# Optimization experiments

Hardware: AMD Instinct MI355X
Metric: run time of the kernel (lower is better)

The kernel has to match this reference:

```python
import jax, jax.numpy as jnp
import numpy as np

D_MODEL = 512
D_STATE = 64
D_CONV = 4
EXPAND = 2
D_INNER = EXPAND * D_MODEL  # 1024
DT_RANK = D_MODEL // 16     # 32 (mamba default: ceil(d_model/16))
BATCH = 1
SEQ = 2048


def setup_inputs() -> dict:
    key = jax.random.key(0)
    ks = jax.random.split(key, 10)
    def n(k, shape, scale):
        return jax.random.normal(k, shape, dtype=jnp.float32) * scale
    x = n(ks[0], (BATCH, SEQ, D_MODEL), 1.0)
    ln_g = jnp.ones((D_MODEL,), jnp.float32)
    ln_b = jnp.zeros((D_MODEL,), jnp.float32)
    Win = n(ks[1], (2 * D_INNER, D_MODEL), D_MODEL ** -0.5)
    conv_w = n(ks[2], (D_INNER, 1, D_CONV), 0.5)      # depthwise kernel (O,I/g,K)
    conv_b = n(ks[3], (D_INNER,), 0.02)
    Wx = n(ks[4], (DT_RANK + 2 * D_STATE, D_INNER), D_INNER ** -0.5)
    Wdt = n(ks[5], (D_INNER, DT_RANK), DT_RANK ** -0.5)
    bdt = n(ks[6], (D_INNER,), 0.02)
    # Mamba S4D-real init: A = 1..d_state repeated per channel
    A_log = jnp.log(jnp.tile(jnp.arange(1, D_STATE + 1, dtype=jnp.float32)[None, :], (D_INNER, 1)))
    Dp = jnp.ones((D_INNER,), jnp.float32)
    Wout = n(ks[7], (D_MODEL, D_INNER), D_INNER ** -0.5)
    return dict(x=x, ln_g=ln_g, ln_b=ln_b, Win=Win, conv_w=conv_w, conv_b=conv_b,
                Wx=Wx, Wdt=Wdt, bdt=bdt, A_log=A_log, Dp=Dp, Wout=Wout)


def _layernorm(x, g, b, eps=1e-5):
    mu = jnp.mean(x, axis=-1, keepdims=True)
    xc = x - mu
    var = jnp.mean(xc * xc, axis=-1, keepdims=True)
    return xc * jax.lax.rsqrt(var + eps) * g + b


def _mamba_block(x, ln_g, ln_b, Win, conv_w, conv_b, Wx, Wdt, bdt, A_log, Dp, Wout):
    residual = x
    xn = _layernorm(x, ln_g, ln_b)
    # in_proj -> (x, z) gates
    xz = jnp.einsum('bld,ed->ble', xn, Win)           # (B,L,2*D_INNER)
    xi, z = jnp.split(xz, 2, axis=-1)
    # causal depthwise conv1d (torch pads d_conv-1 both sides then truncates to L == left-pad only)
    xc = jnp.transpose(xi, (0, 2, 1))                 # (B,C,L)
    xc = jax.lax.conv_general_dilated(
        xc, conv_w, window_strides=(1,), padding=[(D_CONV - 1, 0)],
        dimension_numbers=('NCH', 'OIH', 'NCH'), feature_group_count=D_INNER)
    xc = xc + conv_b[None, :, None]
    xi = jax.nn.silu(jnp.transpose(xc, (0, 2, 1)))    # (B,L,D_INNER)
    # x_proj -> dt, B, C
    dbc = jnp.einsum('bld,ed->ble', xi, Wx)           # (B,L,DT_RANK+2N)
    dt = dbc[..., :DT_RANK]
    Bm = dbc[..., DT_RANK:DT_RANK + D_STATE]          # (B,L,N)
    Cm = dbc[..., DT_RANK + D_STATE:]                 # (B,L,N)
    delta = jax.nn.softplus(jnp.einsum('blr,dr->bld', dt, Wdt) + bdt)  # (B,L,D_INNER)
    A = -jnp.exp(A_log)                               # (D_INNER,N), negative
    dA = jnp.exp(delta[..., None] * A)                # (B,L,D_INNER,N) in (0,1)
    dBx = (delta * xi)[..., None] * Bm[:, :, None, :] # (B,L,D_INNER,N)
    def step(h, t):
        dA_t, dBx_t, C_t = t
        h = dA_t * h + dBx_t                          # (B,D_INNER,N)
        y_t = jnp.einsum('bdn,bn->bd', h, C_t)
        return h, y_t
    h0 = jnp.zeros((x.shape[0], D_INNER, D_STATE), x.dtype)
    _, ys = jax.lax.scan(step, h0, (jnp.transpose(dA, (1, 0, 2, 3)),
                                    jnp.transpose(dBx, (1, 0, 2, 3)),
                                    jnp.transpose(Cm, (1, 0, 2))))
    y = jnp.transpose(ys, (1, 0, 2)) + Dp * xi        # skip term D*x
    y = y * jax.nn.silu(z)                            # gate
    out = jnp.einsum('bld,ed->ble', y, Wout)          # out_proj
    return out + residual


def reference(x, ln_g, ln_b, Win, conv_w, conv_b, Wx, Wdt, bdt, A_log, Dp, Wout):
    return _mamba_block(x, ln_g, ln_b, Win, conv_w, conv_b, Wx, Wdt, bdt, A_log, Dp, Wout)
```

## Files before the change

### kernel.cpp

```cpp
#include <hip/hip_runtime.h>
#include <hip/hip_bf16.h>
#include <cstddef>

#define SEQ 2048
#define DM  512
#define DI  1024
#define DR  32
#define DS  64
#define NCHUNK 32
#define CHUNK  64
#define MB (1024 * 1024)
#define NCVT 1696

typedef __attribute__((ext_vector_type(4))) float f32x4;
typedef __attribute__((ext_vector_type(2))) float f32x2;
typedef __attribute__((ext_vector_type(8))) short frag8;

__device__ __forceinline__ unsigned short f2bf(float f) {
    unsigned u = __float_as_uint(f);
    unsigned r = (u + 0x7fffu + ((u >> 16) & 1u)) >> 16;
    return (unsigned short)r;
}
__device__ __forceinline__ float bf2f(unsigned short u) {
    return __int_as_float(((int)u) << 16);
}

__device__ __forceinline__ float fexp2(float x) {
#if __has_builtin(__builtin_amdgcn_exp2f)
    return __builtin_amdgcn_exp2f(x);
#else
    return exp2f(x);
#endif
}
#define LOG2E 1.44269504088896f

template <int CTRL>
__device__ __forceinline__ f32x2 dppadd2(f32x2 p) {
    f32x2 t;
    t.x = __int_as_float(
        __builtin_amdgcn_update_dpp(0, __float_as_int(p.x), CTRL, 0xF, 0xF, true));
    t.y = __int_as_float(
        __builtin_amdgcn_update_dpp(0, __float_as_int(p.y), CTRL, 0xF, 0xF, true));
    return p + t;
}

__global__ void cvt_ln(const float* __restrict__ w1, unsigned short* __restrict__ o1,
                       const float* __restrict__ w2, unsigned short* __restrict__ o2,
                       const float* __restrict__ w3, unsigned short* __restrict__ o3,
                       const float* __restrict__ x, const float* __restrict__ g,
                       const float* __restrict__ b, unsigned short* __restrict__ xn) {
    if (blockIdx.x < NCVT) {
        const int n1 = 1048576, n2 = 163840, n3 = 524288;
        int i = (blockIdx.x * 256 + threadIdx.x) * 4;
        const float* s; unsigned short* d; int off;
        if (i < n1) { s = w1; d = o1; off = i; }
        else if (i < n1 + n2) { s = w2; d = o2; off = i - n1; }
        else if (i < n1 + n2 + n3) { s = w3; d = o3; off = i - n1 - n2; }
        else return;
        float4 v = *(const float4*)(s + off);
        ushort4 o = { f2bf(v.x), f2bf(v.y), f2bf(v.z), f2bf(v.w) };
        *(ushort4*)(d + off) = o;
        return;
    }
    int l = blockIdx.x - NCVT;
    int t = threadIdx.x;
    __shared__ float red[256];
    float v0 = x[l * DM + t];
    float v1 = x[l * DM + t + 256];
    red[t] = v0 + v1;
    __syncthreads();
    for (int o = 128; o > 0; o >>= 1) { if (t < o) red[t] += red[t + o]; __syncthreads(); }
    float mu = red[0] * (1.f / DM);
    __syncthreads();
    float c0 = v0 - mu, c1 = v1 - mu;
    red[t] = c0 * c0 + c1 * c1;
    __syncthreads();
    for (int o = 128; o > 0; o >>= 1) { if (t < o) red[t] += red[t + o]; __syncthreads(); }
    float rstd = rsqrtf(red[0] * (1.f / DM) + 1e-5f);
    xn[l * DM + t]       = f2bf(c0 * rstd * g[t]       + b[t]);
    xn[l * DM + t + 256] = f2bf(c1 * rstd * g[t + 256] + b[t + 256]);
}

#define LDK 40

template <int EPI>
__global__ __launch_bounds__(256, 2)
void gemm_bf(const unsigned short* __restrict__ A, int lda,
             const unsigned short* __restrict__ B, int ldb,
             int N, int K,
             float* __restrict__ outF, const float* __restrict__ res, int ldo,
             float* __restrict__ dtc, float* __restrict__ Bfp, float* __restrict__ Cfp,
             unsigned short* __restrict__ outB1, unsigned short* __restrict__ outB2) {
    __shared__ unsigned short As[128 * LDK];
    __shared__ unsigned short Bs[64 * LDK];
    int t = threadIdx.x;
    int lane = t & 63;
    int wv = t >> 6;
    int wm = (wv >> 1) * 64;
    int wn = (wv & 1) * 32;
    int m0 = blockIdx.x * 128, n0 = blockIdx.y * 64;

    f32x4 acc[4][2];
#pragma unroll
    for (int i = 0; i < 4; i++)
#pragma unroll
        for (int j = 0; j < 2; j++) acc[i][j] = (f32x4){0.f, 0.f, 0.f, 0.f};

    int lm = lane & 15;
    int kq = (lane >> 4) * 8;

    for (int k0 = 0; k0 < K; k0 += 32) {
#pragma unroll
        for (int j = 0; j < 2; j++) {
            int c = t + j * 256;
            int m = c >> 2;
            int k = (c & 3) * 8;
            frag8 v = *(const frag8*)(A + (size_t)(m0 + m) * lda + k0 + k);
            *(frag8*)(&As[m * LDK + k]) = v;
        }
        {
            int m = t >> 2;
            int k = (t & 3) * 8;
            int gn = n0 + m;
            frag8 v = {0, 0, 0, 0, 0, 0, 0, 0};
            if (gn < N) v = *(const frag8*)(B + (size_t)gn * ldb + k0 + k);
            *(frag8*)(&Bs[m * LDK + k]) = v;
        }
        __syncthreads();

        frag8 af[4], bfr[2];
#pragma unroll
        for (int mt = 0; mt < 4; mt++)
            af[mt] = *(const frag8*)(&As[(wm + mt * 16 + lm) * LDK + kq]);
#pragma unroll
        for (int nt = 0; nt < 2; nt++)
            bfr[nt] = *(const frag8*)(&Bs[(wn + nt * 16 + lm) * LDK + kq]);
#pragma unroll
        for (int mt = 0; mt < 4; mt++)
#pragma unroll
            for (int nt = 0; nt < 2; nt++)
                acc[mt][nt] = __builtin_amdgcn_mfma_f32_16x16x32_bf16(
                    af[mt], bfr[nt], acc[mt][nt], 0, 0, 0);
        __syncthreads();
    }

    int rbase = (lane >> 4) * 4;
#pragma unroll
    for (int mt = 0; mt < 4; mt++) {
#pragma unroll
        for (int nt = 0; nt < 2; nt++) {
            int n = n0 + wn + nt * 16 + lm;
            int mb = m0 + wm + mt * 16 + rbase;
            if (EPI == 1) {
                if (n < DI) {
#pragma unroll
                    for (int r = 0; r < 4; r++)
                        outB1[(size_t)(mb + r) * DI + n] = f2bf(acc[mt][nt][r]);
                } else {
                    int nn = n - DI;
                    ushort4 o;
#pragma unroll
                    for (int r = 0; r < 4; r++) {
                        float v = acc[mt][nt][r];
                        v = v / (1.f + __expf(-v));
                        (&o.x)[r] = f2bf(v);
                    }
                    *(ushort4*)(outB2 + (size_t)nn * SEQ + mb) = o;
                }
            } else if (EPI == 2) {
                if (n < N) {
#pragma unroll
                    for (int r = 0; r < 4; r++)
                        outF[(size_t)(mb + r) * ldo + n] =
                            acc[mt][nt][r] + res[(size_t)(mb + r) * ldo + n];
                }
            } else {
                if (n < 32) {
#pragma unroll
                    for (int r = 0; r < 4; r++)
                        dtc[(size_t)(mb + r) * 32 + n] = acc[mt][nt][r];
                } else if (n < 96) {
#pragma unroll
                    for (int r = 0; r < 4; r++)
                        Bfp[(size_t)(mb + r) * DS + (n - 32)] = acc[mt][nt][r];
                } else if (n < 160) {
#pragma unroll
                    for (int r = 0; r < 4; r++)
                        Cfp[(size_t)(mb + r) * DS + (n - 96)] = acc[mt][nt][r];
                }
            }
        }
    }
}

__global__ void gemm_dt_t(const float* __restrict__ A,
                          const float* __restrict__ B,
                          const float* __restrict__ bias,
                          float* __restrict__ outT) {
    __shared__ float As[16][65];
    __shared__ float Bs[16][65];
    int tid = threadIdx.x;
    int tx = tid & 15, ty = tid >> 4;
    int bm = blockIdx.x * 64, bn = blockIdx.y * 64;
    float acc[4][4] = {};
    int kk = tid & 15;
    int rr = tid >> 4;
    for (int k0 = 0; k0 < DR; k0 += 16) {
#pragma unroll
        for (int i = 0; i < 4; i++)
            As[kk][rr + 16 * i] = A[(size_t)(bm + rr + 16 * i) * 32 + k0 + kk];
#pragma unroll
        for (int i = 0; i < 4; i++)
            Bs[kk][rr + 16 * i] = B[(size_t)(bn + rr + 16 * i) * DR + k0 + kk];
        __syncthreads();
#pragma unroll
        for (int k = 0; k < 16; k++) {
            float a[4], bb[4];
#pragma unroll
            for (int i = 0; i < 4; i++) a[i] = As[k][ty * 4 + i];
#pragma unroll
            for (int j = 0; j < 4; j++) bb[j] = Bs[k][tx * 4 + j];
#pragma unroll
            for (int i = 0; i < 4; i++)
#pragma unroll
                for (int j = 0; j < 4; j++)
                    acc[i][j] = fmaf(a[i], bb[j], acc[i][j]);
        }
        __syncthreads();
    }
#pragma unroll
    for (int j = 0; j < 4; j++) {
        int e = bn + tx * 4 + j;
        float bv = bias[e];
        float4 o;
#pragma unroll
        for (int i = 0; i < 4; i++) {
            float v = acc[i][j] + bv;
            v = (v > 20.f) ? v : __logf(1.f + __expf(v));
            (&o.x)[i] = v;
        }
        *(float4*)(outT + (size_t)e * SEQ + bm + ty * 4) = o;
    }
}

__global__ void conv_t(const unsigned short* __restrict__ xi_raw,
                       const float* __restrict__ w, const float* __restrict__ cb,
                       unsigned short* __restrict__ xi2bf, unsigned short* __restrict__ xi2T) {
    __shared__ float tin[67][72];
    __shared__ float tout[64][65];
    int l0 = blockIdx.x * 64, e0 = blockIdx.y * 64;
    int t = threadIdx.x;
    for (int c = t; c < 536; c += 256) {
        int r = c >> 3, ke = (c & 7) * 8;
        int l = l0 - 3 + r;
        frag8 v = {0, 0, 0, 0, 0, 0, 0, 0};
        if (l >= 0) v = *(const frag8*)(xi_raw + (size_t)l * DI + e0 + ke);
#pragma unroll
        for (int i = 0; i < 8; i++) tin[r][ke + i] = bf2f((unsigned short)v[i]);
    }
    __syncthreads();
    int e_loc = t & 63;
    int e = e0 + e_loc;
    float4 wv = *(const float4*)(w + e * 4);
    float bias = cb[e];
#pragma unroll 4
    for (int i = 0; i < 16; i++) {
        int l_loc = (t >> 6) + i * 4;
        float acc = bias;
        acc = fmaf(wv.x, tin[l_loc][e_loc], acc);
        acc = fmaf(wv.y, tin[l_loc + 1][e_loc], acc);
        acc = fmaf(wv.z, tin[l_loc + 2][e_loc], acc);
        acc = fmaf(wv.w, tin[l_loc + 3][e_loc], acc);
        float s = acc / (1.f + __expf(-acc));
        tout[l_loc][e_loc] = s;
        xi2bf[(size_t)(l0 + l_loc) * DI + e] = f2bf(s);
    }
    __syncthreads();
    for (int c = t; c < 1024; c += 256) {
        int er = c >> 4, l4 = (c & 15) * 4;
        ushort4 o = { f2bf(tout[l4][er]), f2bf(tout[l4 + 1][er]),
                      f2bf(tout[l4 + 2][er]), f2bf(tout[l4 + 3][er]) };
        *(ushort4*)(xi2T + (size_t)(e0 + er) * SEQ + l0 + l4) = o;
    }
}

struct GrpA { float4 dd; ushort4 xx; float4 B[4]; };
struct GrpB { float4 dd; ushort4 xx, zz; float4 B[4], C[4]; };

__device__ __forceinline__ void loadGrpA(GrpA& gr, const float4* d4, const ushort4* x4,
                                         const float4* b4, int gq) {
    gr.dd = d4[gq]; gr.xx = x4[gq];
#pragma unroll
    for (int j = 0; j < 4; j++) gr.B[j] = b4[(4 * gq + j) * 16];
}

__device__ __forceinline__ void loadGrpB(GrpB& gr, const float4* d4, const ushort4* x4,
                                         const ushort4* s4, const float4* b4,
                                         const float4* c4, int gq) {
    gr.dd = d4[gq]; gr.xx = x4[gq]; gr.zz = s4[gq];
#pragma unroll
    for (int j = 0; j < 4; j++) {
        gr.B[j] = b4[(4 * gq + j) * 16];
        gr.C[j] = c4[(4 * gq + j) * 16];
    }
}

__device__ __forceinline__ void compGrpA(const GrpA& gr, f32x2& h01, f32x2& h23,
                                         float& sum_d, f32x2 nA01, f32x2 nA23) {
#pragma unroll
    for (int j = 0; j < 4; j++) {
        float dj = (&gr.dd.x)[j];
        f32x2 dj2 = {dj, dj};
        f32x2 e01 = dj2 * nA01, e23 = dj2 * nA23;
        f32x2 dA01, dA23;
        dA01.x = fexp2(e01.x); dA01.y = fexp2(e01.y);
        dA23.x = fexp2(e23.x); dA23.y = fexp2(e23.y);
        float dx = dj * bf2f((&gr.xx.x)[j]);
        f32x2 dx2 = {dx, dx};
        sum_d += dj;
        f32x2 B01 = {gr.B[j].x, gr.B[j].y}, B23 = {gr.B[j].z, gr.B[j].w};
        h01 = dA01 * h01 + dx2 * B01;
        h23 = dA23 * h23 + dx2 * B23;
    }
}

__device__ __forceinline__ void compGrpB(const GrpB& gr, f32x2& h01, f32x2& h23,
                                         f32x2 nA01, f32x2 nA23, float dp, int i,
                                         size_t ybase, unsigned short* __restrict__ y_bf) {
    float ps[4], xs[4];
#pragma unroll
    for (int j = 0; j < 4; j++) {
        float dj = (&gr.dd.x)[j];
        f32x2 dj2 = {dj, dj};
        f32x2 e01 = dj2 * nA01, e23 = dj2 * nA23;
        f32x2 dA01, dA23;
        dA01.x = fexp2(e01.x); dA01.y = fexp2(e01.y);
        dA23.x = fexp2(e23.x); dA23.y = fexp2(e23.y);
        float xj = bf2f((&gr.xx.x)[j]);
        float dx = dj * xj;
        f32x2 dx2 = {dx, dx};
        f32x2 B01 = {gr.B[j].x, gr.B[j].y}, B23 = {gr.B[j].z, gr.B[j].w};
        h01 = dA01 * h01 + dx2 * B01;
        h23 = dA23 * h23 + dx2 * B23;
        f32x2 C01 = {gr.C[j].x, gr.C[j].y}, C23 = {gr.C[j].z, gr.C[j].w};
        f32x2 pp = h01 * C01;
        pp = h23 * C23 + pp;
        ps[j] = pp.x + pp.y;
        xs[j] = xj;
    }
    f32x2 q01 = {ps[0], ps[1]}, q23 = {ps[2], ps[3]};
    q01 = dppadd2<0xB1>(q01);  q23 = dppadd2<0xB1>(q23);
    q01 = dppadd2<0x4E>(q01);  q23 = dppadd2<0x4E>(q23);
    q01 = dppadd2<0x141>(q01); q23 = dppadd2<0x141>(q23);
    q01 = dppadd2<0x140>(q01); q23 = dppadd2<0x140>(q23);
    f32x2 x01 = {xs[0], xs[1]}, x23 = {xs[2], xs[3]};
    f32x2 z01 = {bf2f(gr.zz.x), bf2f(gr.zz.y)}, z23 = {bf2f(gr.zz.z), bf2f(gr.zz.w)};
    f32x2 dp2 = {dp, dp};
    f32x2 y01 = (q01 + dp2 * x01) * z01;
    f32x2 y23 = (q23 + dp2 * x23) * z23;
    if (i == 0) {
        y_bf[ybase]          = f2bf(y01.x);
        y_bf[ybase + DI]     = f2bf(y01.y);
        y_bf[ybase + 2 * DI] = f2bf(y23.x);
        y_bf[ybase + 3 * DI] = f2bf(y23.y);
    }
}

__global__ __launch_bounds__(256, 4)
void scan_passA(const float* __restrict__ deltaT, const unsigned short* __restrict__ xi2T,
                const float* __restrict__ Bf, const float* __restrict__ A_log,
                float* __restrict__ sumd, float* __restrict__ hend) {
    __shared__ float Bsh[CHUNK * DS];
    int t = threadIdx.x;
    int wid = blockIdx.x * 4 + (t >> 6);
    int eg = wid & 255;
    int c  = wid >> 8;
    int l0 = c * CHUNK;
#pragma unroll
    for (int it = 0; it < 4; it++) {
        int idx = (it * 256 + t) * 4;
        *(float4*)&Bsh[idx] = *(const float4*)(Bf + (size_t)l0 * DS + idx);
    }
    __syncthreads();
    int lane = t & 63;
    int g = lane >> 4;
    int i = lane & 15;
    int e = eg * 4 + g;
    float4 al = *(const float4*)(A_log + e * DS + 4 * i);
    f32x2 nA01 = { -__expf(al.x) * LOG2E, -__expf(al.y) * LOG2E };
    f32x2 nA23 = { -__expf(al.z) * LOG2E, -__expf(al.w) * LOG2E };
    f32x2 h01 = {0.f, 0.f}, h23 = {0.f, 0.f};
    float sum_d = 0.f;
    const float4* d4  = (const float4*)(deltaT + (size_t)e * SEQ + l0);
    const ushort4* x4 = (const ushort4*)(xi2T + (size_t)e * SEQ + l0);
    const float4* b4  = (const float4*)Bsh + i;
    GrpA ga, gb;
    loadGrpA(ga, d4, x4, b4, 0);
    for (int p = 0; p < CHUNK / 8; p++) {
        loadGrpA(gb, d4, x4, b4, 2 * p + 1);
        compGrpA(ga, h01, h23, sum_d, nA01, nA23);
        if (p < CHUNK / 8 - 1) loadGrpA(ga, d4, x4, b4, 2 * p + 2);
        compGrpA(gb, h01, h23, sum_d, nA01, nA23);
    }
    size_t idx = ((size_t)c * DI + e) * DS + 4 * i;
    float4 hv = {h01.x, h01.y, h23.x, h23.y};
    *(float4*)(hend + idx) = hv;
    if (i == 0) sumd[c * DI + e] = sum_d;
}

__global__ void scan_carry(float* __restrict__ hend, const float* __restrict__ sumd,
                           const float* __restrict__ A_log) {
    int e = blockIdx.x * 4 + (threadIdx.x >> 6);
    int n = threadIdx.x & 63;
    float Ae2 = -__expf(A_log[e * DS + n]) * LOG2E;
    float he[NCHUNK - 1], sd[NCHUNK - 1];
#pragma unroll
    for (int c = 0; c < NCHUNK - 1; c++)
        he[c] = hend[((size_t)c * DI + e) * DS + n];
#pragma unroll
    for (int c = 0; c < NCHUNK - 1; c++)
        sd[c] = sumd[c * DI + e];
    float h = 0.f;
#pragma unroll
    for (int c = 0; c < NCHUNK - 1; c++) {
        float P = fexp2(Ae2 * sd[c]);
        hend[((size_t)c * DI + e) * DS + n] = h;
        h = fmaf(P, h, he[c]);
    }
    hend[((size_t)(NCHUNK - 1) * DI + e) * DS + n] = h;
}

__global__ __launch_bounds__(256, 4)
void scan_passB(const float* __restrict__ deltaT, const unsigned short* __restrict__ xi2T,
                const float* __restrict__ Bf, const float* __restrict__ Cf,
                const unsigned short* __restrict__ szT,
                const float* __restrict__ A_log, const float* __restrict__ Dp,
                const float* __restrict__ hin, unsigned short* __restrict__ y_bf) {
    __shared__ float Bsh[CHUNK * DS];
    __shared__ float Csh[CHUNK * DS];
    int t = threadIdx.x;
    int wid = blockIdx.x * 4 + (t >> 6);
    int eg = wid & 255;
    int c  = wid >> 8;
    int l0 = c * CHUNK;
#pragma unroll
    for (int it = 0; it < 4; it++) {
        int idx = (it * 256 + t) * 4;
        *(float4*)&Bsh[idx] = *(const float4*)(Bf + (size_t)l0 * DS + idx);
        *(float4*)&Csh[idx] = *(const float4*)(Cf + (size_t)l0 * DS + idx);
    }
    __syncthreads();
    int lane = t & 63;
    int g = lane >> 4;
    int i = lane & 15;
    int e = eg * 4 + g;
    float4 al = *(const float4*)(A_log + e * DS + 4 * i);
    f32x2 nA01 = { -__expf(al.x) * LOG2E, -__expf(al.y) * LOG2E };
    f32x2 nA23 = { -__expf(al.z) * LOG2E, -__expf(al.w) * LOG2E };
    float dp = Dp[e];
    float4 hv = *(const float4*)(hin + ((size_t)c * DI + e) * DS + 4 * i);
    f32x2 h01 = {hv.x, hv.y}, h23 = {hv.z, hv.w};
    const float4* d4  = (const float4*)(deltaT + (size_t)e * SEQ + l0);
    const ushort4* x4 = (const ushort4*)(xi2T + (size_t)e * SEQ + l0);
    const ushort4* s4 = (const ushort4*)(szT + (size_t)e * SEQ + l0);
    const float4* b4  = (const float4*)Bsh + i;
    const float4* c4  = (const float4*)Csh + i;
    size_t ybase = (size_t)l0 * DI + e;
    GrpB ga, gb;
    loadGrpB(ga, d4, x4, s4, b4, c4, 0);
    for (int p = 0; p < CHUNK / 8; p++) {
        loadGrpB(gb, d4, x4, s4, b4, c4, 2 * p + 1);
        compGrpB(ga, h01, h23, nA01, nA23, dp, i, ybase + (size_t)(8 * p) * DI, y_bf);
        if (p < CHUNK / 8 - 1) loadGrpB(ga, d4, x4, s4, b4, c4, 2 * p + 2);
        compGrpB(gb, h01, h23, nA01, nA23, dp, i, ybase + (size_t)(8 * p + 4) * DI, y_bf);
    }
}

extern "C" void kernel_launch(void* const* d_in, const int* in_sizes, int n_in,
                              void* d_out, int out_size, void* d_ws, size_t ws_size,
                              hipStream_t stream) {
    const float* x      = (const float*)d_in[0];
    const float* ln_g   = (const float*)d_in[1];
    const float* ln_b   = (const float*)d_in[2];
    const float* Win    = (const float*)d_in[3];
    const float* conv_w = (const float*)d_in[4];
    const float* conv_b = (const float*)d_in[5];
    const float* Wx     = (const float*)d_in[6];
    const float* Wdt    = (const float*)d_in[7];
    const float* bdt    = (const float*)d_in[8];
    const float* A_log  = (const float*)d_in[9];
    const float* Dp     = (const float*)d_in[10];
    const float* Wout   = (const float*)d_in[11];
    float* out = (float*)d_out;

    char* W = (char*)d_ws;
    unsigned short* xi_raw  = (unsigned short*)W;
    float*          deltaT  = (float*)W;
    unsigned short* Win_bf  = (unsigned short*)(W + 8 * MB);
    unsigned short* xi2bf   = (unsigned short*)(W + 8 * MB);
    unsigned short* y_bf    = (unsigned short*)(W + 8 * MB);
    unsigned short* szT     = (unsigned short*)(W + 12 * MB);
    unsigned short* xi2T    = (unsigned short*)(W + 16 * MB);
    unsigned short* xn_bf   = (unsigned short*)(W + 20 * MB);
    float*          hend    = (float*)(W + 20 * MB);
    unsigned short* Wout_bf = (unsigned short*)(W + 28 * MB);
    float*          sumd    = (float*)(W + 29 * MB);
    unsigned short* Wx_bf   = (unsigned short*)(W + 29 * MB + 128 * 1024);
    float*          dtc     = (float*)(W + 29 * MB + 448 * 1024);
    float*          Bf      = (float*)(W + 29 * MB + 704 * 1024);
    float*          Cf      = Bf + (size_t)SEQ * DS;

    cvt_ln<<<NCVT + SEQ, 256, 0, stream>>>(Win, Win_bf, Wx, Wx_bf, Wout, Wout_bf,
                                           x, ln_g, ln_b, xn_bf);

    gemm_bf<1><<<dim3(SEQ / 128, 2048 / 64), 256, 0, stream>>>(
        xn_bf, DM, Win_bf, DM, 2048, DM, nullptr, nullptr, 0, nullptr, nullptr, nullptr,
        xi_raw, szT);

    conv_t<<<dim3(SEQ / 64, DI / 64), 256, 0, stream>>>(xi_raw, conv_w, conv_b, xi2bf, xi2T);

    gemm_bf<4><<<dim3(SEQ / 128, 3), 256, 0, stream>>>(
        xi2bf, DI, Wx_bf, DI, 160, DI, nullptr, nullptr, 0, dtc, Bf, Cf, nullptr, nullptr);

    gemm_dt_t<<<dim3(SEQ / 64, DI / 64), 256, 0, stream>>>(dtc, Wdt, bdt, deltaT);

    scan_passA<<<(DI / 4) * (NCHUNK - 1) / 4, 256, 0, stream>>>(deltaT, xi2T, Bf, A_log, sumd, hend);
    scan_carry<<<DI / 4, 256, 0, stream>>>(hend, sumd, A_log);
    scan_passB<<<(DI / 4) * NCHUNK / 4, 256, 0, stream>>>(deltaT, xi2T, Bf, Cf, szT,
                                                          A_log, Dp, hend, y_bf);

    gemm_bf<2><<<dim3(SEQ / 128, DM / 64), 256, 0, stream>>>(
        y_bf, DI, Wout_bf, DI, DM, DI, out, x, DM, nullptr, nullptr, nullptr,
        nullptr, nullptr);
}
```

Measured before the change: 219.7 us.

## Double-buffer GEMM tiles with direct global-to-LDS loads and pad Wx weights

The bf16 GEMM now stages A and B tiles straight from global memory into LDS with global_load_lds, using two LDS buffers so the next K-slice loads while MFMAs run on the current one. This drops the VGPR round trip and one barrier per iteration. To remove the N bound check on B, the Wx weight copy is zero-padded from 160 to 192 rows, and the conversion grid and workspace offsets grow to fit. The unpadded LDS layout (stride 32) may raise bank conflicts on fragment reads.

```diff
diff --git a/kernel.cpp b/kernel.cpp
--- a/kernel.cpp
+++ b/kernel.cpp
@@ -10,7 +10,7 @@
 #define NCHUNK 32
 #define CHUNK  64
 #define MB (1024 * 1024)
-#define NCVT 1696
+#define NCVT 1728
 
 typedef __attribute__((ext_vector_type(4))) float f32x4;
 typedef __attribute__((ext_vector_type(2))) float f32x2;
@@ -33,6 +33,12 @@
 #endif
 }
 #define LOG2E 1.44269504088896f
+
+__device__ __forceinline__ void gld16(const void* g, void* l) {
+    __builtin_amdgcn_global_load_lds(
+        (const __attribute__((address_space(1))) unsigned int*)g,
+        (__attribute__((address_space(3))) unsigned int*)l, 16, 0, 0);
+}
 
 template <int CTRL>
 __device__ __forceinline__ f32x2 dppadd2(f32x2 p) {
@@ -50,14 +56,15 @@
                        const float* __restrict__ x, const float* __restrict__ g,
                        const float* __restrict__ b, unsigned short* __restrict__ xn) {
     if (blockIdx.x < NCVT) {
-        const int n1 = 1048576, n2 = 163840, n3 = 524288;
+        const int n1 = 1048576, n2 = 196608, n3 = 524288;
         int i = (blockIdx.x * 256 + threadIdx.x) * 4;
-        const float* s; unsigned short* d; int off;
+        const float* s; unsigned short* d; int off; int lim = 1 << 30;
         if (i < n1) { s = w1; d = o1; off = i; }
-        else if (i < n1 + n2) { s = w2; d = o2; off = i - n1; }
+        else if (i < n1 + n2) { s = w2; d = o2; off = i - n1; lim = 163840; }
         else if (i < n1 + n2 + n3) { s = w3; d = o3; off = i - n1 - n2; }
         else return;
-        float4 v = *(const float4*)(s + off);
+        float4 v = {0.f, 0.f, 0.f, 0.f};
+        if (off < lim) v = *(const float4*)(s + off);
         ushort4 o = { f2bf(v.x), f2bf(v.y), f2bf(v.z), f2bf(v.w) };
         *(ushort4*)(d + off) = o;
         return;
@@ -81,7 +88,7 @@
     xn[l * DM + t + 256] = f2bf(c1 * rstd * g[t + 256] + b[t + 256]);
 }
 
-#define LDK 40
+#define BK 32
 
 template <int EPI>
 __global__ __launch_bounds__(256, 2)
@@ -91,8 +98,8 @@
              float* __restrict__ outF, const float* __restrict__ res, int ldo,
              float* __restrict__ dtc, float* __restrict__ Bfp, float* __restrict__ Cfp,
              unsigned short* __restrict__ outB1, unsigned short* __restrict__ outB2) {
-    __shared__ unsigned short As[128 * LDK];
-    __shared__ unsigned short Bs[64 * LDK];
+    __shared__ unsigned short As[2][128 * BK];
+    __shared__ unsigned short Bs[2][64 * BK];
     int t = threadIdx.x;
     int lane = t & 63;
     int wv = t >> 6;
@@ -109,32 +116,29 @@
     int lm = lane & 15;
     int kq = (lane >> 4) * 8;
 
-    for (int k0 = 0; k0 < K; k0 += 32) {
-#pragma unroll
-        for (int j = 0; j < 2; j++) {
-            int c = t + j * 256;
-            int m = c >> 2;
-            int k = (c & 3) * 8;
-            frag8 v = *(const frag8*)(A + (size_t)(m0 + m) * lda + k0 + k);
-            *(frag8*)(&As[m * LDK + k]) = v;
+    int am = t >> 2, ak = (t & 3) * 8;
+    const unsigned short* gA0 = A + (size_t)(m0 + am) * lda + ak;
+    const unsigned short* gA1 = A + (size_t)(m0 + am + 64) * lda + ak;
+    const unsigned short* gB  = B + (size_t)(n0 + am) * ldb + ak;
+
+    gld16(gA0, &As[0][8 * t]);
+    gld16(gA1, &As[0][8 * t + 64 * BK]);
+    gld16(gB,  &Bs[0][8 * t]);
+    __syncthreads();
+    int cur = 0;
+    for (int k0 = 0; k0 < K; k0 += BK) {
+        if (k0 + BK < K) {
+            gld16(gA0 + k0 + BK, &As[cur ^ 1][8 * t]);
+            gld16(gA1 + k0 + BK, &As[cur ^ 1][8 * t + 64 * BK]);
+            gld16(gB + k0 + BK,  &Bs[cur ^ 1][8 * t]);
         }
-        {
-            int m = t >> 2;
-            int k = (t & 3) * 8;
-            int gn = n0 + m;
-            frag8 v = {0, 0, 0, 0, 0, 0, 0, 0};
-            if (gn < N) v = *(const frag8*)(B + (size_t)gn * ldb + k0 + k);
-            *(frag8*)(&Bs[m * LDK + k]) = v;
-        }
-        __syncthreads();
-
         frag8 af[4], bfr[2];
 #pragma unroll
         for (int mt = 0; mt < 4; mt++)
-            af[mt] = *(const frag8*)(&As[(wm + mt * 16 + lm) * LDK + kq]);
+            af[mt] = *(const frag8*)(&As[cur][(wm + mt * 16 + lm) * BK + kq]);
 #pragma unroll
         for (int nt = 0; nt < 2; nt++)
-            bfr[nt] = *(const frag8*)(&Bs[(wn + nt * 16 + lm) * LDK + kq]);
+            bfr[nt] = *(const frag8*)(&Bs[cur][(wn + nt * 16 + lm) * BK + kq]);
 #pragma unroll
         for (int mt = 0; mt < 4; mt++)
 #pragma unroll
@@ -142,6 +146,7 @@
                 acc[mt][nt] = __builtin_amdgcn_mfma_f32_16x16x32_bf16(
                     af[mt], bfr[nt], acc[mt][nt], 0, 0, 0);
         __syncthreads();
+        cur ^= 1;
     }
 
     int rbase = (lane >> 4) * 4;
@@ -506,8 +511,8 @@
     unsigned short* Wout_bf = (unsigned short*)(W + 28 * MB);
     float*          sumd    = (float*)(W + 29 * MB);
     unsigned short* Wx_bf   = (unsigned short*)(W + 29 * MB + 128 * 1024);
-    float*          dtc     = (float*)(W + 29 * MB + 448 * 1024);
-    float*          Bf      = (float*)(W + 29 * MB + 704 * 1024);
+    float*          dtc     = (float*)(W + 29 * MB + 512 * 1024);
+    float*          Bf      = (float*)(W + 29 * MB + 768 * 1024);
     float*          Cf      = Bf + (size_t)SEQ * DS;
 
     cvt_ln<<<NCVT + SEQ, 256, 0, stream>>>(Win, Win_bf, Wx, Wx_bf, Wout, Wout_bf,
@@ -520,7 +525,7 @@
     conv_t<<<dim3(SEQ / 64, DI / 64), 256, 0, stream>>>(xi_raw, conv_w, conv_b, xi2bf, xi2T);
 
     gemm_bf<4><<<dim3(SEQ / 128, 3), 256, 0, stream>>>(
-        xi2bf, DI, Wx_bf, DI, 160, DI, nullptr, nullptr, 0, dtc, Bf, Cf, nullptr, nullptr);
+        xi2bf, DI, Wx_bf, DI, 192, DI, nullptr, nullptr, 0, dtc, Bf, Cf, nullptr, nullptr);
 
     gemm_dt_t<<<dim3(SEQ / 64, DI / 64), 256, 0, stream>>>(dtc, Wdt, bdt, deltaT);
 
```

Result: faster. 207.3 us (-5.6%).
